# Kernel tuning notes

Measured on AMD Instinct MI355X. Metric: run time of the kernel, lower is better.

The kernel has to match this reference:

```python
import math
import jax, jax.numpy as jnp
import numpy as np

B, T, D, H = 2, 2048, 1024, 16
N_LAYERS = 24


def get_slopes(n):
    def pow2(n):
        start = 2 ** (-2 ** (-(math.log2(n) - 3)))
        return [start * start ** i for i in range(n)]
    if math.log2(n).is_integer():
        return pow2(n)
    c = 2 ** math.floor(math.log2(n))
    return pow2(c) + get_slopes(2 * c)[0::2][: n - c]


def setup_inputs() -> dict:
    key = jax.random.key(0)
    ks = jax.random.split(key, 5)
    x = jax.random.normal(ks[0], (B, T, D), dtype=jnp.float32)
    Wq = 0.02 * jax.random.normal(ks[1], (D, D), dtype=jnp.float32)
    Wk = 0.02 * jax.random.normal(ks[2], (D, D), dtype=jnp.float32)
    Wv = 0.02 * jax.random.normal(ks[3], (D, D), dtype=jnp.float32)
    Wo = (0.02 / math.sqrt(2 * N_LAYERS)) * jax.random.normal(ks[4], (D, D), dtype=jnp.float32)
    z = jnp.zeros((D,), dtype=jnp.float32)
    return {"x": x, "Wq": Wq, "bq": z, "Wk": Wk, "bk": z, "Wv": Wv, "bv": z, "Wo": Wo, "bo": z}


def reference(x, Wq, bq, Wk, bk, Wv, bv, Wo, bo):
    Bb, Tt, C = x.shape
    hd = C // H
    # QKV projections -> (B, H, T, hd)
    q = (x @ Wq + bq).reshape(Bb, Tt, H, hd).transpose(0, 2, 1, 3)
    k = (x @ Wk + bk).reshape(Bb, Tt, H, hd).transpose(0, 2, 1, 3)
    v = (x @ Wv + bv).reshape(Bb, Tt, H, hd).transpose(0, 2, 1, 3)
    # scaled dot-product scores (B, H, T, T)
    attn = jnp.einsum('bhqd,bhkd->bhqk', q, k) / jnp.sqrt(jnp.asarray(hd, x.dtype))
    # ALiBi bias: module uses only last row of the relative-position matrix,
    # broadcast over query positions: -slope_h * (T-1 - j), shape (1, H, 1, T)
    slopes = jnp.asarray(get_slopes(H), dtype=x.dtype)
    alibi = -slopes[None, :, None, None] * (Tt - 1 - jnp.arange(Tt, dtype=x.dtype))[None, None, None, :]
    attn = attn + alibi
    # causal mask
    causal = jnp.tril(jnp.ones((Tt, Tt), dtype=bool))[None, None, :, :]
    attn = jnp.where(causal, attn, jnp.finfo(x.dtype).min)
    p = jax.nn.softmax(attn, axis=-1)
    out = jnp.einsum('bhqk,bhkd->bqhd', p, v).reshape(Bb, Tt, C)
    return out @ Wo + bo
```

## Files before the change

kernel.cpp:

```cpp
#include <hip/hip_runtime.h>
#include <hip/hip_bf16.h>

#define Bn 2
#define Tdim 2048
#define Ddim 1024
#define Hn 16
#define HD 64

typedef unsigned short u16;
typedef unsigned int u32;
typedef __attribute__((ext_vector_type(8))) __bf16 bf16x8;
typedef __attribute__((ext_vector_type(4))) float f32x4;
typedef __attribute__((ext_vector_type(16))) float f32x16;
typedef __attribute__((ext_vector_type(4))) u32 u32x4;

struct alignas(8) U16x4 { u16 x, y, z, w; };

__device__ __forceinline__ u16 f2bf(float f) {
  union { float f; u32 i; } v; v.f = f;
  u32 x = v.i;
  u32 r = (x + 0x7fffu + ((x >> 16) & 1u)) >> 16;
  return (u16)r;
}
__device__ __forceinline__ float bf2f(u16 u) {
  union { u32 i; float f; } v; v.i = ((u32)u) << 16; return v.f;
}

__device__ __forceinline__ u32 cvtpk_bf16(float a, float b) {
  u32 d;
  asm("v_cvt_pk_bf16_f32 %0, %1, %2" : "=v"(d) : "v"(a), "v"(b));
  return d;
}

__device__ __forceinline__ void cp16(const u16* g, u16* l) {
  __builtin_amdgcn_global_load_lds(
      (const __attribute__((address_space(1))) u32*)g,
      (__attribute__((address_space(3))) u32*)l, 16, 0, 0);
}

__device__ __forceinline__ f32x4 mfma16(bf16x8 a, bf16x8 b, f32x4 c) {
  return __builtin_amdgcn_mfma_f32_16x16x32_bf16(a, b, c, 0, 0, 0);
}
__device__ __forceinline__ f32x16 mfma32(bf16x8 a, bf16x8 b, f32x16 c) {
  return __builtin_amdgcn_mfma_f32_32x32x16_bf16(a, b, c, 0, 0, 0);
}

__global__ __launch_bounds__(256) void convert_x(const float* __restrict__ src,
                                                 u16* __restrict__ dst) {
  const int i = (blockIdx.x * 256 + threadIdx.x) * 8;
  u16 t[8];
#pragma unroll
  for (int j = 0; j < 8; j++) t[j] = f2bf(src[i + j]);
  *(bf16x8*)&dst[i] = *(const bf16x8*)t;
}

__global__ __launch_bounds__(256) void transpose_k(
    const float* __restrict__ s0, const float* __restrict__ s1,
    const float* __restrict__ s2, const float* __restrict__ s3,
    u16* __restrict__ dst) {
  const float* src = (blockIdx.z == 0) ? s0 : (blockIdx.z == 1) ? s1
                   : (blockIdx.z == 2) ? s2 : s3;
  u16* d = dst + (size_t)blockIdx.z * Ddim * Ddim;
  __shared__ u16 tile[32][33];
  const int tx = threadIdx.x, ty = threadIdx.y;
  const int x = blockIdx.x * 32 + tx;
  const int y0 = blockIdx.y * 32;
#pragma unroll
  for (int j = 0; j < 32; j += 8) tile[ty + j][tx] = f2bf(src[(size_t)(y0 + ty + j) * Ddim + x]);
  __syncthreads();
  const int xo = blockIdx.y * 32 + tx;
  const int yo0 = blockIdx.x * 32;
#pragma unroll
  for (int j = 0; j < 32; j += 8) d[(size_t)(yo0 + ty + j) * Ddim + xo] = tile[tx][ty + j];
}

__global__ __launch_bounds__(256, 2) void gemm_qkv(
    const u16* __restrict__ Xb, const u16* __restrict__ WT,
    const float* __restrict__ bq, const float* __restrict__ bk, const float* __restrict__ bv,
    u16* __restrict__ Q, u16* __restrict__ K, u16* __restrict__ Vt) {
  const int flat = blockIdx.x + 32 * (blockIdx.y + 8 * blockIdx.z);
  const int l = (flat & 7) * 96 + (flat >> 3);
  const int lbx = l & 31, lby = (l >> 5) & 7, z = l >> 8;

  const u16* Wt = WT + (size_t)z * Ddim * Ddim;
  const float* bias = (z == 0) ? bq : (z == 1) ? bk : bv;
  u16* QK = (z == 0) ? Q : K;

  __shared__ alignas(16) u16 Alds[128 * 64];
  __shared__ alignas(16) u16 Blds[128 * 64];
  const int tid = threadIdx.x;
  const int w = tid >> 6, lane = tid & 63, ln = lane & 15, quad = lane >> 4;
  const int wm = (w >> 1) * 64, wn = (w & 1) * 64;
  const int tm = lbx * 128, tn = lby * 128;

  f32x4 acc[4][4] = {};

  const int srow = lane >> 3;
  const int scol = ((lane & 7) ^ srow) * 8;
  const u16* ag0 = Xb + (size_t)(tm + w * 32 + srow) * Ddim + scol;
  const u16* bg0 = Wt + (size_t)(tn + w * 32 + srow) * Ddim + scol;

  for (int k0 = 0; k0 < Ddim; k0 += 64) {
    __syncthreads();
#pragma unroll
    for (int j = 0; j < 4; j++) {
      cp16(ag0 + (size_t)j * 8 * Ddim + k0, &Alds[(w * 32 + j * 8) * 64]);
      cp16(bg0 + (size_t)j * 8 * Ddim + k0, &Blds[(w * 32 + j * 8) * 64]);
    }
    __syncthreads();
#pragma unroll
    for (int k2 = 0; k2 < 2; k2++) {
      const int so = ((k2 * 4 + quad) ^ (ln & 7)) * 8;
      bf16x8 af[4], bfr[4];
#pragma unroll
      for (int i = 0; i < 4; i++)
        af[i] = *(const bf16x8*)&Alds[(wm + i * 16 + ln) * 64 + so];
#pragma unroll
      for (int i = 0; i < 4; i++)
        bfr[i] = *(const bf16x8*)&Blds[(wn + i * 16 + ln) * 64 + so];
#pragma unroll
      for (int mi = 0; mi < 4; mi++)
#pragma unroll
        for (int ni = 0; ni < 4; ni++)
          acc[mi][ni] = mfma16(af[mi], bfr[ni], acc[mi][ni]);
    }
  }

#pragma unroll
  for (int mi = 0; mi < 4; mi++) {
#pragma unroll
    for (int ni = 0; ni < 4; ni++) {
      const int gm0 = tm + wm + mi * 16 + quad * 4;
      const int gn = tn + wn + ni * 16 + ln;
      const float bv_ = bias[gn];
      const int hh = gn >> 6, dd = gn & 63;
      const int b0 = gm0 >> 11, t0 = gm0 & 2047;
      if (z < 2) {
        u16* p = QK + (((size_t)(b0 * Hn + hh) * Tdim) + t0) * HD + dd;
#pragma unroll
        for (int r = 0; r < 4; r++) p[r * HD] = f2bf(acc[mi][ni][r] + bv_);
      } else {
        U16x4 pk;
        pk.x = f2bf(acc[mi][ni][0] + bv_);
        pk.y = f2bf(acc[mi][ni][1] + bv_);
        pk.z = f2bf(acc[mi][ni][2] + bv_);
        pk.w = f2bf(acc[mi][ni][3] + bv_);
        *(U16x4*)&Vt[((size_t)(b0 * Hn + hh) * HD + dd) * Tdim + t0] = pk;
      }
    }
  }
}

#define KSTR 68
#define VSTR 132
#define L2E 1.44269504088896f
__global__ __launch_bounds__(256, 2) void attn_k(
    const u16* __restrict__ Q, const u16* __restrict__ K, const u16* __restrict__ Vt,
    u16* __restrict__ Op, float* __restrict__ lp) {
  __shared__ alignas(16) u16 Klds[128 * KSTR];
  __shared__ alignas(16) u16 Vtlds[64 * VSTR];

  const int id = blockIdx.x;
  const int xcd = id & 7, slot = id >> 3;
  const int bh = (xcd << 2) | (slot >> 4);
  const int inner = slot & 15;
  const int p = inner >> 1;
  const int s = inner & 1;
  const int tid = threadIdx.x;
  const int w = tid >> 6, lane = tid & 63;
  const int qi = lane & 31, hf = lane >> 5;

  const u16* Qh = Q + (size_t)bh * Tdim * HD;
  const u16* Kh = K + (size_t)bh * Tdim * HD;
  const u16* Vh = Vt + (size_t)bh * HD * Tdim;
  const float slope = exp2f(-0.5f * (float)((bh & 15) + 1));

  const float sl2 = slope * L2E;
  const float c1 = 0.125f * L2E;
  const float f4hf = (float)(4 * hf);
  float sg8[4], slm[4];
#pragma unroll
  for (int g = 0; g < 4; g++) sg8[g] = sl2 * (float)(8 * g);
#pragma unroll
  for (int m = 0; m < 4; m++) slm[m] = sl2 * (float)m;

  const int qbs[2] = {p, 15 - p};
  int K0[2], K1[2];
#pragma unroll
  for (int seg = 0; seg < 2; seg++) {
    const int nk = qbs[seg] + 1;
    const int h0 = (nk + 1) >> 1;
    K0[seg] = s ? h0 : 0;
    K1[seg] = s ? nk : h0;
  }

  bf16x8 kreg[4], vreg[4];
  {
    const int kb = ((K0[0] < K1[0]) ? K0[0] : K0[1]) * 128;
#pragma unroll
    for (int c = 0; c < 4; c++) {
      const int e = c * 2048 + tid * 8;
      kreg[c] = *(const bf16x8*)&Kh[(size_t)(kb + (e >> 6)) * HD + (e & 63)];
      vreg[c] = *(const bf16x8*)&Vh[(size_t)(e >> 7) * Tdim + kb + (e & 127)];
    }
  }

  for (int seg = 0; seg < 2; seg++) {
    const int qb = qbs[seg];
    const int kt0 = K0[seg], kt1 = K1[seg];
    const int nkt = qb + 1;
    const int q0 = qb * 128;
    const int tg = q0 + w * 32 + qi;
    const float tt2 = (slope * (float)tg + 3.0f) * L2E;

    bf16x8 qf[4];
#pragma unroll
    for (int kc = 0; kc < 4; kc++)
      qf[kc] = *(const bf16x8*)&Qh[(size_t)tg * HD + kc * 16 + hf * 8];

    float ls0 = 0.f, ls1 = 0.f;
    f32x16 oacc[2] = {};

    for (int kt = kt0; kt < kt1; kt++) {
      const int kb = kt * 128;
      __syncthreads();
#pragma unroll
      for (int c = 0; c < 4; c++) {
        const int e = c * 2048 + tid * 8;
        *(bf16x8*)&Klds[(e >> 6) * KSTR + (e & 63)] = kreg[c];
        *(bf16x8*)&Vtlds[(e >> 7) * VSTR + (e & 127)] = vreg[c];
      }
      __syncthreads();

      {
        const int nxt = (kt + 1 < kt1) ? (kt + 1) : ((seg == 0) ? K0[1] : -1);
        if (nxt >= 0) {
          const int kb2 = nxt * 128;
#pragma unroll
          for (int c = 0; c < 4; c++) {
            const int e = c * 2048 + tid * 8;
            kreg[c] = *(const bf16x8*)&Kh[(size_t)(kb2 + (e >> 6)) * HD + (e & 63)];
            vreg[c] = *(const bf16x8*)&Vh[(size_t)(e >> 7) * Tdim + kb2 + (e & 127)];
          }
        }
      }

      f32x16 st[4] = {};
      __builtin_amdgcn_s_setprio(1);
#pragma unroll
      for (int kc = 0; kc < 4; kc++) {
#pragma unroll
        for (int ni = 0; ni < 4; ni++) {
          bf16x8 kf = *(const bf16x8*)&Klds[(ni * 32 + qi) * KSTR + kc * 16 + hf * 8];
          st[ni] = mfma32(kf, qf[kc], st[ni]);
        }
      }
      __builtin_amdgcn_s_setprio(0);

      const bool diag = (kt == nkt - 1);
      const float fkb = (float)kb + f4hf;
      bf16x8 pfrag[8];
#pragma unroll
      for (int ni = 0; ni < 4; ni++) {
        const float cni = __builtin_fmaf(sl2, fkb + (float)(32 * ni), -tt2);
        float pv[16];
        if (!diag) {
#pragma unroll
          for (int ri = 0; ri < 16; ri++) {
            const float e = __builtin_fmaf(st[ni][ri], c1, cni + sg8[ri >> 2] + slm[ri & 3]);
            const float pp = __builtin_amdgcn_exp2f(e);
            if (ri & 1) ls1 += pp; else ls0 += pp;
            pv[ri] = pp;
          }
        } else {
#pragma unroll
          for (int ri = 0; ri < 16; ri++) {
            const int n = kb + ni * 32 + (ri & 3) + 8 * (ri >> 2) + 4 * hf;
            const float e = __builtin_fmaf(st[ni][ri], c1, cni + sg8[ri >> 2] + slm[ri & 3]);
            float pp = __builtin_amdgcn_exp2f(e);
            if (n > tg) pp = 0.f;
            if (ri & 1) ls1 += pp; else ls0 += pp;
            pv[ri] = pp;
          }
        }
        u32 pk[4][2];
#pragma unroll
        for (int g = 0; g < 4; g++) {
          pk[g][0] = cvtpk_bf16(pv[g * 4 + 0], pv[g * 4 + 1]);
          pk[g][1] = cvtpk_bf16(pv[g * 4 + 2], pv[g * 4 + 3]);
        }
#pragma unroll
        for (int a = 0; a < 2; a++) {
          const u32 snd0 = (hf == 0) ? pk[2 * a + 1][0] : pk[2 * a][0];
          const u32 snd1 = (hf == 0) ? pk[2 * a + 1][1] : pk[2 * a][1];
          const u32 rcv0 = (u32)__shfl_xor((int)snd0, 32);
          const u32 rcv1 = (u32)__shfl_xor((int)snd1, 32);
          u32x4 fr;
          fr.x = (hf == 0) ? pk[2 * a][0] : rcv0;
          fr.y = (hf == 0) ? pk[2 * a][1] : rcv1;
          fr.z = (hf == 0) ? rcv0 : pk[2 * a + 1][0];
          fr.w = (hf == 0) ? rcv1 : pk[2 * a + 1][1];
          pfrag[ni * 2 + a] = *(bf16x8*)&fr;
        }
      }

      __builtin_amdgcn_s_setprio(1);
#pragma unroll
      for (int kf16 = 0; kf16 < 8; kf16++) {
#pragma unroll
        for (int nd = 0; nd < 2; nd++) {
          bf16x8 vf = *(const bf16x8*)&Vtlds[(nd * 32 + qi) * VSTR + kf16 * 16 + hf * 8];
          oacc[nd] = mfma32(pfrag[kf16], vf, oacc[nd]);
        }
      }
      __builtin_amdgcn_s_setprio(0);
    }

    float lsum = ls0 + ls1;
    lsum += __shfl_xor(lsum, 32);
    if (hf == 0) lp[(size_t)s * 65536 + bh * Tdim + tg] = lsum;

    u16* Ob = Op + (size_t)s * (32u * Tdim * HD) + ((size_t)bh * Tdim) * HD;
#pragma unroll
    for (int nd = 0; nd < 2; nd++) {
#pragma unroll
      for (int ri = 0; ri < 16; ri++) {
        const int rq = (ri & 3) + 8 * (ri >> 2) + 4 * hf;
        const int t = q0 + w * 32 + rq;
        Ob[(size_t)t * HD + nd * 32 + qi] = f2bf(oacc[nd][ri]);
      }
    }
  }
}

__global__ __launch_bounds__(256) void merge_k(const u16* __restrict__ Op,
                                               const float* __restrict__ lp,
                                               u16* __restrict__ AO) {
  const int i = blockIdx.x * 256 + threadIdx.x;
  const int d8 = i & 7;
  const int t = (i >> 3) & 2047;
  const int bh = i >> 14;
  const int b = bh >> 4, h = bh & 15;
  const float l = lp[bh * Tdim + t] + lp[65536 + bh * Tdim + t];
  const float inv = 1.0f / l;
  const size_t off = ((size_t)bh * Tdim + t) * HD + d8 * 8;
  const u16* O0 = Op + off;
  const u16* O1 = Op + (size_t)32 * Tdim * HD + off;
  u16 outv[8];
#pragma unroll
  for (int j = 0; j < 8; j++)
    outv[j] = f2bf((bf2f(O0[j]) + bf2f(O1[j])) * inv);
  *(bf16x8*)&AO[((size_t)(b * Tdim + t)) * Ddim + h * HD + d8 * 8] = *(const bf16x8*)outv;
}

__global__ __launch_bounds__(256, 2) void gemm_out(
    const u16* __restrict__ A, const u16* __restrict__ WoT, const float* __restrict__ bo,
    float* __restrict__ C) {
  const int flat = blockIdx.x + 64 * blockIdx.y;
  const int l = (flat & 7) * 64 + (flat >> 3);
  const int lbx = l & 63, lby = l >> 6;

  __shared__ alignas(16) u16 Alds[64 * 64];
  __shared__ alignas(16) u16 Blds[128 * 64];
  const int tid = threadIdx.x;
  const int w = tid >> 6, lane = tid & 63, ln = lane & 15, quad = lane >> 4;
  const int tm = lbx * 64, tn = lby * 128;

  f32x4 acc[4][2] = {};

  const int srow = lane >> 3;
  const int scol = ((lane & 7) ^ srow) * 8;
  const u16* ag0 = A + (size_t)(tm + w * 16 + srow) * Ddim + scol;
  const u16* bg0 = WoT + (size_t)(tn + w * 32 + srow) * Ddim + scol;

  for (int k0 = 0; k0 < Ddim; k0 += 64) {
    __syncthreads();
#pragma unroll
    for (int j = 0; j < 2; j++)
      cp16(ag0 + (size_t)j * 8 * Ddim + k0, &Alds[(w * 16 + j * 8) * 64]);
#pragma unroll
    for (int j = 0; j < 4; j++)
      cp16(bg0 + (size_t)j * 8 * Ddim + k0, &Blds[(w * 32 + j * 8) * 64]);
    __syncthreads();
#pragma unroll
    for (int k2 = 0; k2 < 2; k2++) {
      const int so = ((k2 * 4 + quad) ^ (ln & 7)) * 8;
      bf16x8 af[4], bfr[2];
#pragma unroll
      for (int i = 0; i < 4; i++)
        af[i] = *(const bf16x8*)&Alds[(i * 16 + ln) * 64 + so];
#pragma unroll
      for (int i = 0; i < 2; i++)
        bfr[i] = *(const bf16x8*)&Blds[(w * 32 + i * 16 + ln) * 64 + so];
#pragma unroll
      for (int mi = 0; mi < 4; mi++)
#pragma unroll
        for (int ni = 0; ni < 2; ni++)
          acc[mi][ni] = mfma16(af[mi], bfr[ni], acc[mi][ni]);
    }
  }

#pragma unroll
  for (int mi = 0; mi < 4; mi++) {
#pragma unroll
    for (int ni = 0; ni < 2; ni++) {
      const int gm0 = tm + mi * 16 + quad * 4;
      const int gn = tn + w * 32 + ni * 16 + ln;
      const float bv_ = bo[gn];
#pragma unroll
      for (int r = 0; r < 4; r++)
        C[(size_t)(gm0 + r) * Ddim + gn] = acc[mi][ni][r] + bv_;
    }
  }
}

extern "C" void kernel_launch(void* const* d_in, const int* in_sizes, int n_in,
                              void* d_out, int out_size, void* d_ws, size_t ws_size,
                              hipStream_t stream) {
  (void)in_sizes; (void)n_in; (void)out_size; (void)ws_size;
  const float* x  = (const float*)d_in[0];
  const float* Wq = (const float*)d_in[1];
  const float* bq = (const float*)d_in[2];
  const float* Wk = (const float*)d_in[3];
  const float* bk = (const float*)d_in[4];
  const float* Wv = (const float*)d_in[5];
  const float* bv = (const float*)d_in[6];
  const float* Wo = (const float*)d_in[7];
  const float* bo = (const float*)d_in[8];

  char* ws = (char*)d_ws;
  const size_t MB = 1024 * 1024;
  u16* WT   = (u16*)(ws + 0 * MB);
  u16* Qb   = (u16*)(ws + 8 * MB);
  u16* Kb   = (u16*)(ws + 16 * MB);
  u16* Vtb  = (u16*)(ws + 24 * MB);
  u16* Xb   = (u16*)(ws + 32 * MB);
  u16* AO   = (u16*)(ws + 32 * MB);
  u16* Opart= (u16*)(ws + 40 * MB);
  float* lpart = (float*)(ws + 56 * MB);
  u16* WoT = WT + (size_t)3 * Ddim * Ddim;

  convert_x<<<dim3(2048), 256, 0, stream>>>(x, Xb);
  transpose_k<<<dim3(32, 32, 4), dim3(32, 8), 0, stream>>>(Wq, Wk, Wv, Wo, WT);

  gemm_qkv<<<dim3(32, 8, 3), 256, 0, stream>>>(Xb, WT, bq, bk, bv, Qb, Kb, Vtb);
  attn_k<<<dim3(512), 256, 0, stream>>>(Qb, Kb, Vtb, Opart, lpart);
  merge_k<<<dim3(2048), 256, 0, stream>>>(Opart, lpart, AO);
  gemm_out<<<dim3(64, 8), 256, 0, stream>>>(AO, WoT, bo, (float*)d_out);
}
```

Measured before the change: 182.7 us.

## Fuse split-K attention merge into output GEMM and merge preprocessing kernels

The merge of the two split attention partials (sum and divide by the combined softmax denominator) now happens inside the output-projection GEMM's A-tile load, so the merge kernel and its intermediate buffer are gone. The x conversion and weight transposes are combined into one launch as an extra grid slice. Together these remove two kernel launches and a full write and read of the attention output. In exchange, each of the 8 column-block tiles of gemm_out redoes the merge for the same rows, so partial loads and reciprocals are repeated. The A loads also become synchronous register loads instead of async global-to-LDS copies.

```diff
diff --git a/kernel.cpp b/kernel.cpp
--- a/kernel.cpp
+++ b/kernel.cpp
@@ -45,28 +45,32 @@
   return __builtin_amdgcn_mfma_f32_32x32x16_bf16(a, b, c, 0, 0, 0);
 }
 
-__global__ __launch_bounds__(256) void convert_x(const float* __restrict__ src,
-                                                 u16* __restrict__ dst) {
-  const int i = (blockIdx.x * 256 + threadIdx.x) * 8;
-  u16 t[8];
-#pragma unroll
-  for (int j = 0; j < 8; j++) t[j] = f2bf(src[i + j]);
-  *(bf16x8*)&dst[i] = *(const bf16x8*)t;
-}
-
-__global__ __launch_bounds__(256) void transpose_k(
+__global__ __launch_bounds__(256) void preproc_k(
+    const float* __restrict__ x, u16* __restrict__ Xb,
     const float* __restrict__ s0, const float* __restrict__ s1,
     const float* __restrict__ s2, const float* __restrict__ s3,
-    u16* __restrict__ dst) {
+    u16* __restrict__ dstW) {
+  const int tx = threadIdx.x, ty = threadIdx.y;
+  if (blockIdx.z == 4) {
+    const int tid = ty * 32 + tx;
+    const int i = ((blockIdx.y * 32 + blockIdx.x) * 256 + tid) * 16;
+#pragma unroll
+    for (int c = 0; c < 2; c++) {
+      u16 t[8];
+#pragma unroll
+      for (int j = 0; j < 8; j++) t[j] = f2bf(x[i + c * 8 + j]);
+      *(bf16x8*)&Xb[i + c * 8] = *(const bf16x8*)t;
+    }
+    return;
+  }
   const float* src = (blockIdx.z == 0) ? s0 : (blockIdx.z == 1) ? s1
                    : (blockIdx.z == 2) ? s2 : s3;
-  u16* d = dst + (size_t)blockIdx.z * Ddim * Ddim;
+  u16* d = dstW + (size_t)blockIdx.z * Ddim * Ddim;
   __shared__ u16 tile[32][33];
-  const int tx = threadIdx.x, ty = threadIdx.y;
-  const int x = blockIdx.x * 32 + tx;
+  const int xx = blockIdx.x * 32 + tx;
   const int y0 = blockIdx.y * 32;
 #pragma unroll
-  for (int j = 0; j < 32; j += 8) tile[ty + j][tx] = f2bf(src[(size_t)(y0 + ty + j) * Ddim + x]);
+  for (int j = 0; j < 32; j += 8) tile[ty + j][tx] = f2bf(src[(size_t)(y0 + ty + j) * Ddim + xx]);
   __syncthreads();
   const int xo = blockIdx.y * 32 + tx;
   const int yo0 = blockIdx.x * 32;
@@ -333,28 +337,9 @@
   }
 }
 
-__global__ __launch_bounds__(256) void merge_k(const u16* __restrict__ Op,
-                                               const float* __restrict__ lp,
-                                               u16* __restrict__ AO) {
-  const int i = blockIdx.x * 256 + threadIdx.x;
-  const int d8 = i & 7;
-  const int t = (i >> 3) & 2047;
-  const int bh = i >> 14;
-  const int b = bh >> 4, h = bh & 15;
-  const float l = lp[bh * Tdim + t] + lp[65536 + bh * Tdim + t];
-  const float inv = 1.0f / l;
-  const size_t off = ((size_t)bh * Tdim + t) * HD + d8 * 8;
-  const u16* O0 = Op + off;
-  const u16* O1 = Op + (size_t)32 * Tdim * HD + off;
-  u16 outv[8];
-#pragma unroll
-  for (int j = 0; j < 8; j++)
-    outv[j] = f2bf((bf2f(O0[j]) + bf2f(O1[j])) * inv);
-  *(bf16x8*)&AO[((size_t)(b * Tdim + t)) * Ddim + h * HD + d8 * 8] = *(const bf16x8*)outv;
-}
-
 __global__ __launch_bounds__(256, 2) void gemm_out(
-    const u16* __restrict__ A, const u16* __restrict__ WoT, const float* __restrict__ bo,
+    const u16* __restrict__ Op, const float* __restrict__ lp,
+    const u16* __restrict__ WoT, const float* __restrict__ bo,
     float* __restrict__ C) {
   const int flat = blockIdx.x + 64 * blockIdx.y;
   const int l = (flat & 7) * 64 + (flat >> 3);
@@ -370,17 +355,45 @@
 
   const int srow = lane >> 3;
   const int scol = ((lane & 7) ^ srow) * 8;
-  const u16* ag0 = A + (size_t)(tm + w * 16 + srow) * Ddim + scol;
   const u16* bg0 = WoT + (size_t)(tn + w * 32 + srow) * Ddim + scol;
 
+  const int ar = tid >> 3;
+  const int ac8 = tid & 7;
+  const int row0 = tm + ar, row1 = tm + ar + 32;
+  const int b0r = row0 >> 11, t0r = row0 & 2047;
+  const int b1r = row1 >> 11, t1r = row1 & 2047;
+  const size_t pstr = (size_t)32 * Tdim * HD;
+  const int aslot = (ac8 ^ (ar & 7)) * 8;
+
   for (int k0 = 0; k0 < Ddim; k0 += 64) {
+    const int h = k0 >> 6;
     __syncthreads();
-#pragma unroll
-    for (int j = 0; j < 2; j++)
-      cp16(ag0 + (size_t)j * 8 * Ddim + k0, &Alds[(w * 16 + j * 8) * 64]);
 #pragma unroll
     for (int j = 0; j < 4; j++)
       cp16(bg0 + (size_t)j * 8 * Ddim + k0, &Blds[(w * 32 + j * 8) * 64]);
+    {
+      const int bh0 = b0r * Hn + h, bh1 = b1r * Hn + h;
+      const size_t o0 = ((size_t)bh0 * Tdim + t0r) * HD + ac8 * 8;
+      const size_t o1 = ((size_t)bh1 * Tdim + t1r) * HD + ac8 * 8;
+      const u32x4 a00 = *(const u32x4*)&Op[o0];
+      const u32x4 a01 = *(const u32x4*)&Op[pstr + o0];
+      const u32x4 a10 = *(const u32x4*)&Op[o1];
+      const u32x4 a11 = *(const u32x4*)&Op[pstr + o1];
+      const float inv0 = 1.0f / (lp[bh0 * Tdim + t0r] + lp[65536 + bh0 * Tdim + t0r]);
+      const float inv1 = 1.0f / (lp[bh1 * Tdim + t1r] + lp[65536 + bh1 * Tdim + t1r]);
+      u32x4 q0, q1;
+#pragma unroll
+      for (int jj = 0; jj < 4; jj++) {
+        const float lo0 = bf2f((u16)(a00[jj] & 0xffffu)) + bf2f((u16)(a01[jj] & 0xffffu));
+        const float hi0 = bf2f((u16)(a00[jj] >> 16)) + bf2f((u16)(a01[jj] >> 16));
+        q0[jj] = cvtpk_bf16(lo0 * inv0, hi0 * inv0);
+        const float lo1 = bf2f((u16)(a10[jj] & 0xffffu)) + bf2f((u16)(a11[jj] & 0xffffu));
+        const float hi1 = bf2f((u16)(a10[jj] >> 16)) + bf2f((u16)(a11[jj] >> 16));
+        q1[jj] = cvtpk_bf16(lo1 * inv1, hi1 * inv1);
+      }
+      *(u32x4*)&Alds[ar * 64 + aslot] = q0;
+      *(u32x4*)&Alds[(ar + 32) * 64 + aslot] = q1;
+    }
     __syncthreads();
 #pragma unroll
     for (int k2 = 0; k2 < 2; k2++) {
@@ -435,16 +448,12 @@
   u16* Kb   = (u16*)(ws + 16 * MB);
   u16* Vtb  = (u16*)(ws + 24 * MB);
   u16* Xb   = (u16*)(ws + 32 * MB);
-  u16* AO   = (u16*)(ws + 32 * MB);
   u16* Opart= (u16*)(ws + 40 * MB);
   float* lpart = (float*)(ws + 56 * MB);
   u16* WoT = WT + (size_t)3 * Ddim * Ddim;
 
-  convert_x<<<dim3(2048), 256, 0, stream>>>(x, Xb);
-  transpose_k<<<dim3(32, 32, 4), dim3(32, 8), 0, stream>>>(Wq, Wk, Wv, Wo, WT);
-
+  preproc_k<<<dim3(32, 32, 5), dim3(32, 8), 0, stream>>>(x, Xb, Wq, Wk, Wv, Wo, WT);
   gemm_qkv<<<dim3(32, 8, 3), 256, 0, stream>>>(Xb, WT, bq, bk, bv, Qb, Kb, Vtb);
   attn_k<<<dim3(512), 256, 0, stream>>>(Qb, Kb, Vtb, Opart, lpart);
-  merge_k<<<dim3(2048), 256, 0, stream>>>(Opart, lpart, AO);
-  gemm_out<<<dim3(64, 8), 256, 0, stream>>>(AO, WoT, bo, (float*)d_out);
-}
+  gemm_out<<<dim3(64, 8), 256, 0, stream>>>(Opart, lpart, WoT, bo, (float*)d_out);
+}
```

After: 191.8 us. 1.05x slower.
